# Kernel optimization log

Measured on AMD Instinct MI355X. Metric: run time of the kernel, lower is better.

## Reference

```python
import jax, jax.numpy as jnp
import numpy as np

N_NODES = 100000


def _gcn_norm(edge_index, num_nodes):
    # Add self-loops, then symmetric normalization D^-1/2 A D^-1/2 (PyG gcn_norm).
    loops = jnp.arange(num_nodes, dtype=edge_index.dtype)
    src = jnp.concatenate([edge_index[0], loops])
    dst = jnp.concatenate([edge_index[1], loops])
    ew = jnp.ones(src.shape[0], dtype=jnp.float32)
    deg = jax.ops.segment_sum(ew, dst, num_segments=num_nodes)
    dinv = jnp.where(deg > 0, jax.lax.rsqrt(deg), 0.0)
    norm = dinv[src] * ew * dinv[dst]
    return src, dst, norm


def _prop_gcn_conv(x, W, b, src, dst, norm, num_nodes, prop_nums):
    # PropGCNConv: linear transform once, then prop_nums hops of normalized
    # sparse propagation (gather from src, scale, scatter-add to dst), + bias.
    x = x @ W
    for _ in range(prop_nums):
        msgs = x[src] * norm[:, None]              # [E, d]
        x = jax.ops.segment_sum(msgs, dst, num_segments=num_nodes)
    return x + b


def setup_inputs() -> dict:
    key = jax.random.key(0)
    k1, k2, k3, k4 = jax.random.split(key, 4)
    in_dim, hid_dim, num_classes = 128, 64, 40
    n_edges = 800000
    x = jax.random.normal(k1, (N_NODES, in_dim), dtype=jnp.float32)
    W0 = jax.random.normal(k2, (in_dim, hid_dim), dtype=jnp.float32) * (1.0 / np.sqrt(in_dim))
    b0 = jnp.zeros((hid_dim,), dtype=jnp.float32)
    Wc = jax.random.normal(k3, (hid_dim, num_classes), dtype=jnp.float32) * (1.0 / np.sqrt(hid_dim))
    bc = jnp.zeros((num_classes,), dtype=jnp.float32)
    edge_index = jax.random.randint(k4, (2, n_edges), 0, N_NODES, dtype=jnp.int64)
    return {"x": x, "W0": W0, "b0": b0, "Wc": Wc, "bc": bc,
            "edge_index": edge_index, "prop_nums": 30}


def reference(x, W0, b0, Wc, bc, edge_index, prop_nums):
    n = x.shape[0]
    src, dst, norm = _gcn_norm(edge_index, n)
    # feat_bottleneck: conv -> relu -> dropout (eval mode -> identity)
    h = _prop_gcn_conv(x, W0, b0, src, dst, norm, n, prop_nums)
    h = jax.nn.relu(h)
    # feat_classifier: single-hop PropGCNConv
    out = _prop_gcn_conv(h, Wc, bc, src, dst, norm, n, 1)
    return out
```

## Files before the change

### kernel.cpp

```cpp
#include <hip/hip_runtime.h>

#define NN  100000
#define NE  800000
#define NNZ 900000
#define IN_DIM 128
#define HID 64
#define NC  40
#define HOPS 30
#define PB  2048
#define NPAIR (NN / 2)

typedef _Float16 half8 __attribute__((ext_vector_type(8)));


__global__ void count_edges_k(const int* __restrict__ dst, int* __restrict__ cnt) {
    int e = blockIdx.x * blockDim.x + threadIdx.x;
    if (e < NE) atomicAdd(&cnt[dst[e]], 1);
}

__global__ void dinv_k(const int* __restrict__ cnt, float* __restrict__ dinv) {
    int i = blockIdx.x * blockDim.x + threadIdx.x;
    if (i < NN) dinv[i] = rsqrtf((float)(cnt[i] + 1));
}

__global__ void scan_blocks_k(const int* __restrict__ cnt, int* __restrict__ rp,
                              int* __restrict__ partials) {
    __shared__ int s[256];
    int tid = threadIdx.x;
    int i = blockIdx.x * 256 + tid;
    int v = (i < NN) ? (cnt[i] + 1) : 0;
    s[tid] = v;
    __syncthreads();
    for (int off = 1; off < 256; off <<= 1) {
        int t = (tid >= off) ? s[tid - off] : 0;
        __syncthreads();
        s[tid] += t;
        __syncthreads();
    }
    if (i < NN) rp[i] = s[tid] - v;
    if (tid == 255) partials[blockIdx.x] = s[255];
}

__global__ void scan_partials_k(int* __restrict__ partials, int nblk) {
    __shared__ int s[512];
    int tid = threadIdx.x;
    int v = (tid < nblk) ? partials[tid] : 0;
    s[tid] = v;
    __syncthreads();
    for (int off = 1; off < 512; off <<= 1) {
        int t = (tid >= off) ? s[tid - off] : 0;
        __syncthreads();
        s[tid] += t;
        __syncthreads();
    }
    if (tid < nblk) partials[tid] = s[tid] - v;
}

__global__ void add_offsets_k(int* __restrict__ rp, const int* __restrict__ partials) {
    int i = blockIdx.x * 256 + threadIdx.x;
    if (i < NN) rp[i] += partials[blockIdx.x];
    if (i == 0) rp[NN] = NNZ;
}

__global__ void fill_csr_k(const int* __restrict__ src, const int* __restrict__ dst,
                           const float* __restrict__ dinv, const int* __restrict__ rp,
                           int* __restrict__ cnt, int2* __restrict__ cv) {
    int e = blockIdx.x * blockDim.x + threadIdx.x;
    if (e >= NNZ) return;
    int pos;
    int2 p;
    if (e < NE) {
        int s = src[e], d = dst[e];
        int old = atomicAdd(&cnt[d], -1);
        pos = rp[d] + old - 1;
        p.x = s;
        p.y = __float_as_int(dinv[s] * dinv[d]);
    } else {
        int i = e - NE;
        pos = rp[i + 1] - 1;
        p.x = i;
        p.y = __float_as_int(dinv[i] * dinv[i]);
    }
    cv[pos] = p;
}


__global__ void __launch_bounds__(256) gemm1_k(const float* __restrict__ x,
                                               const float* __restrict__ W,
                                               _Float16* __restrict__ out) {
    int t = threadIdx.x;
    int cq = __builtin_amdgcn_readfirstlane(t >> 6);
    int node = blockIdx.x * 64 + (t & 63);
    int nc = node < NN ? node : NN - 1;
    const float4* xr = (const float4*)(x + (size_t)nc * IN_DIM);
    const float* Wq = W + cq * 16;
    float acc[16];
#pragma unroll
    for (int c = 0; c < 16; ++c) acc[c] = 0.f;
#pragma unroll 4
    for (int k4 = 0; k4 < IN_DIM / 4; ++k4) {
        float4 xv = xr[k4];
#pragma unroll
        for (int kk = 0; kk < 4; ++kk) {
            float xs = (kk == 0) ? xv.x : (kk == 1) ? xv.y : (kk == 2) ? xv.z : xv.w;
            const float4* wr = (const float4*)(Wq + (k4 * 4 + kk) * HID);
#pragma unroll
            for (int c4 = 0; c4 < 4; ++c4) {
                float4 wv = wr[c4];
                acc[c4 * 4 + 0] = fmaf(xs, wv.x, acc[c4 * 4 + 0]);
                acc[c4 * 4 + 1] = fmaf(xs, wv.y, acc[c4 * 4 + 1]);
                acc[c4 * 4 + 2] = fmaf(xs, wv.z, acc[c4 * 4 + 2]);
                acc[c4 * 4 + 3] = fmaf(xs, wv.w, acc[c4 * 4 + 3]);
            }
        }
    }
    if (node < NN) {
        half8* o = (half8*)(out + (size_t)node * HID + cq * 16);
        half8 r0, r1;
#pragma unroll
        for (int j = 0; j < 8; ++j) {
            r0[j] = (_Float16)acc[j];
            r1[j] = (_Float16)acc[j + 8];
        }
        o[0] = r0;
        o[1] = r1;
    }
}

__global__ void __launch_bounds__(256) prop64_k(const _Float16* __restrict__ xin,
                                                _Float16* __restrict__ xout,
                                                const int* __restrict__ rp,
                                                const int2* __restrict__ cv) {
    int w    = (blockIdx.x * 256 + threadIdx.x) >> 6;
    int lane = threadIdx.x & 63;
    int n    = lane >> 5;
    int s    = (lane >> 3) & 3;
    int f    = lane & 7;
    const int NW = PB * 4;
    const half8* x8 = (const half8*)xin;
    for (int p = w; p < NPAIR; p += NW) {
        int node = p * 2 + n;
        int beg = rp[node], end = rp[node + 1];
        float a0 = 0.f, a1 = 0.f, a2 = 0.f, a3 = 0.f,
              a4 = 0.f, a5 = 0.f, a6 = 0.f, a7 = 0.f;
        for (int e = beg + s; e < end; e += 16) {
            int  e1 = e + 4,  e2 = e + 8,  e3 = e + 12;
            bool p1 = e1 < end, p2 = e2 < end, p3 = e3 < end;
            int2 q0 = cv[e];
            int2 q1 = cv[p1 ? e1 : beg];
            int2 q2 = cv[p2 ? e2 : beg];
            int2 q3 = cv[p3 ? e3 : beg];
            float v0 = __int_as_float(q0.y);
            float v1 = p1 ? __int_as_float(q1.y) : 0.f;
            float v2 = p2 ? __int_as_float(q2.y) : 0.f;
            float v3 = p3 ? __int_as_float(q3.y) : 0.f;
            half8 x0 = x8[(size_t)q0.x * 8 + f];
            half8 x1 = x8[(size_t)q1.x * 8 + f];
            half8 x2 = x8[(size_t)q2.x * 8 + f];
            half8 x3 = x8[(size_t)q3.x * 8 + f];
            a0 += v0 * (float)x0[0] + v1 * (float)x1[0] + v2 * (float)x2[0] + v3 * (float)x3[0];
            a1 += v0 * (float)x0[1] + v1 * (float)x1[1] + v2 * (float)x2[1] + v3 * (float)x3[1];
            a2 += v0 * (float)x0[2] + v1 * (float)x1[2] + v2 * (float)x2[2] + v3 * (float)x3[2];
            a3 += v0 * (float)x0[3] + v1 * (float)x1[3] + v2 * (float)x2[3] + v3 * (float)x3[3];
            a4 += v0 * (float)x0[4] + v1 * (float)x1[4] + v2 * (float)x2[4] + v3 * (float)x3[4];
            a5 += v0 * (float)x0[5] + v1 * (float)x1[5] + v2 * (float)x2[5] + v3 * (float)x3[5];
            a6 += v0 * (float)x0[6] + v1 * (float)x1[6] + v2 * (float)x2[6] + v3 * (float)x3[6];
            a7 += v0 * (float)x0[7] + v1 * (float)x1[7] + v2 * (float)x2[7] + v3 * (float)x3[7];
        }
#pragma unroll
        for (int m = 8; m <= 16; m <<= 1) {
            a0 += __shfl_xor(a0, m); a1 += __shfl_xor(a1, m);
            a2 += __shfl_xor(a2, m); a3 += __shfl_xor(a3, m);
            a4 += __shfl_xor(a4, m); a5 += __shfl_xor(a5, m);
            a6 += __shfl_xor(a6, m); a7 += __shfl_xor(a7, m);
        }
        if (s == 0) {
            half8 r;
            r[0] = (_Float16)a0; r[1] = (_Float16)a1; r[2] = (_Float16)a2; r[3] = (_Float16)a3;
            r[4] = (_Float16)a4; r[5] = (_Float16)a5; r[6] = (_Float16)a6; r[7] = (_Float16)a7;
            ((half8*)xout)[(size_t)node * 8 + f] = r;
        }
    }
}

__global__ void __launch_bounds__(256, 4) gemm2_k(const _Float16* __restrict__ h,
                                                  const float* __restrict__ b0,
                                                  const float* __restrict__ Wc,
                                                  _Float16* __restrict__ g) {
    __shared__ float Wcs[HID * NC];
    __shared__ float b0s[HID];
    int t = threadIdx.x;
    for (int i = t; i < HID * NC / 4; i += 256)
        ((float4*)Wcs)[i] = ((const float4*)Wc)[i];
    if (t < HID) b0s[t] = b0[t];
    __syncthreads();
    int node = blockIdx.x * 256 + t;
    if (node >= NN) return;
    const half8* hr = (const half8*)(h + (size_t)node * HID);
    float acc[NC];
#pragma unroll
    for (int c = 0; c < NC; ++c) acc[c] = 0.f;
#pragma unroll
    for (int j = 0; j < 8; ++j) {
        half8 hv = hr[j];
#pragma unroll
        for (int m = 0; m < 8; ++m) {
            int k = j * 8 + m;
            float fv = fmaxf((float)hv[m] + b0s[k], 0.f);
            const float4* wr = (const float4*)(Wcs + k * NC);
#pragma unroll
            for (int c4 = 0; c4 < NC / 4; ++c4) {
                float4 wv = wr[c4];
                acc[c4 * 4 + 0] = fmaf(fv, wv.x, acc[c4 * 4 + 0]);
                acc[c4 * 4 + 1] = fmaf(fv, wv.y, acc[c4 * 4 + 1]);
                acc[c4 * 4 + 2] = fmaf(fv, wv.z, acc[c4 * 4 + 2]);
                acc[c4 * 4 + 3] = fmaf(fv, wv.w, acc[c4 * 4 + 3]);
            }
        }
    }
    half8* go = (half8*)(g + (size_t)node * NC);
#pragma unroll
    for (int j = 0; j < 5; ++j) {
        half8 r;
#pragma unroll
        for (int m = 0; m < 8; ++m) r[m] = (_Float16)acc[j * 8 + m];
        go[j] = r;
    }
}

__global__ void __launch_bounds__(256) prop40_k(const _Float16* __restrict__ g,
                                                float* __restrict__ out,
                                                const int* __restrict__ rp,
                                                const int2* __restrict__ cv,
                                                const float* __restrict__ bc) {
    int w    = (blockIdx.x * 256 + threadIdx.x) >> 6;
    int lane = threadIdx.x & 63;
    int s = lane >> 3;
    int f = lane & 7;
    const int NW = PB * 4;
    const half8* g8 = (const half8*)g;
    bool act = f < 5;
    for (int node = w; node < NN; node += NW) {
        int beg = rp[node], end = rp[node + 1];
        float a0 = 0.f, a1 = 0.f, a2 = 0.f, a3 = 0.f, a4 = 0.f, a5 = 0.f, a6 = 0.f, a7 = 0.f;
        for (int e = beg + s; e < end; e += 16) {
            int  e1 = e + 8;
            bool p1 = e1 < end;
            int2 q0 = cv[e];
            int2 q1 = cv[p1 ? e1 : beg];
            float v0 = __int_as_float(q0.y);
            float v1 = p1 ? __int_as_float(q1.y) : 0.f;
            if (act) {
                half8 x0 = g8[(size_t)q0.x * 5 + f];
                half8 x1 = g8[(size_t)q1.x * 5 + f];
                a0 += v0 * (float)x0[0] + v1 * (float)x1[0];
                a1 += v0 * (float)x0[1] + v1 * (float)x1[1];
                a2 += v0 * (float)x0[2] + v1 * (float)x1[2];
                a3 += v0 * (float)x0[3] + v1 * (float)x1[3];
                a4 += v0 * (float)x0[4] + v1 * (float)x1[4];
                a5 += v0 * (float)x0[5] + v1 * (float)x1[5];
                a6 += v0 * (float)x0[6] + v1 * (float)x1[6];
                a7 += v0 * (float)x0[7] + v1 * (float)x1[7];
            }
        }
#pragma unroll
        for (int m = 8; m <= 32; m <<= 1) {
            a0 += __shfl_xor(a0, m); a1 += __shfl_xor(a1, m);
            a2 += __shfl_xor(a2, m); a3 += __shfl_xor(a3, m);
            a4 += __shfl_xor(a4, m); a5 += __shfl_xor(a5, m);
            a6 += __shfl_xor(a6, m); a7 += __shfl_xor(a7, m);
        }
        if (s == 0 && act) {
            float* o = out + (size_t)node * NC + f * 8;
            o[0] = a0 + bc[f * 8 + 0];
            o[1] = a1 + bc[f * 8 + 1];
            o[2] = a2 + bc[f * 8 + 2];
            o[3] = a3 + bc[f * 8 + 3];
            o[4] = a4 + bc[f * 8 + 4];
            o[5] = a5 + bc[f * 8 + 5];
            o[6] = a6 + bc[f * 8 + 6];
            o[7] = a7 + bc[f * 8 + 7];
        }
    }
}


extern "C" void kernel_launch(void* const* d_in, const int* in_sizes, int n_in,
                              void* d_out, int out_size, void* d_ws, size_t ws_size,
                              hipStream_t stream) {
    const float* x  = (const float*)d_in[0];
    const float* W0 = (const float*)d_in[1];
    const float* b0 = (const float*)d_in[2];
    const float* Wc = (const float*)d_in[3];
    const float* bc = (const float*)d_in[4];
    const int*   ei = (const int*)d_in[5];
    const int* src = ei;
    const int* dst = ei + NE;

    char* ws = (char*)d_ws;
    size_t off = 0;
    auto alloc = [&](size_t bytes) -> void* {
        void* p = ws + off;
        off = (off + bytes + 255) & ~(size_t)255;
        return p;
    };
    float* dinv     = (float*)alloc((size_t)NN * 4);
    int*   rp       = (int*)  alloc((size_t)(NN + 1) * 4);
    int*   cnt      = (int*)  alloc((size_t)NN * 4);
    int*   partials = (int*)  alloc(512 * 4);
    int2*  cvp      = (int2*) alloc((size_t)NNZ * 8);
    _Float16* XA    = (_Float16*)alloc((size_t)NN * HID * 2);
    _Float16* XB    = (_Float16*)alloc((size_t)NN * HID * 2);
    _Float16* G     = (_Float16*)alloc((size_t)NN * NC * 2);

    const int nblk_n = (NN + 255) / 256;

    hipMemsetAsync(cnt, 0, (size_t)NN * 4, stream);
    count_edges_k<<<(NE + 255) / 256, 256, 0, stream>>>(dst, cnt);
    dinv_k       <<<nblk_n, 256, 0, stream>>>(cnt, dinv);
    scan_blocks_k<<<nblk_n, 256, 0, stream>>>(cnt, rp, partials);
    scan_partials_k<<<1, 512, 0, stream>>>(partials, nblk_n);
    add_offsets_k<<<nblk_n, 256, 0, stream>>>(rp, partials);
    fill_csr_k   <<<(NNZ + 255) / 256, 256, 0, stream>>>(src, dst, dinv, rp, cnt, cvp);

    gemm1_k<<<(NN + 63) / 64, 256, 0, stream>>>(x, W0, XA);

    _Float16* a = XA;
    _Float16* b = XB;
    for (int hop = 0; hop < HOPS; ++hop) {
        prop64_k<<<PB, 256, 0, stream>>>(a, b, rp, cvp);
        _Float16* tmp = a; a = b; b = tmp;
    }

    gemm2_k<<<nblk_n, 256, 0, stream>>>(a, b0, Wc, G);
    prop40_k<<<PB, 256, 0, stream>>>(G, (float*)d_out, rp, cvp, bc);
}
```

Before: 880.3 us.

## Split hidden features into four 16-wide planes for cache-friendly propagation

Hidden activations move from node-major 64-wide rows to four feature-quarter planes of 16 halves each. Each propagation block handles one quarter, so the random gathers within a block hit a 3.2 MB plane that can stay cache resident. Block IDs are interleaved across quarters. Edge reads and output writes now use nontemporal hints, and gemm2 is reworked to read the new layout. In exchange, the CSR edge list is read four times per hop and each gather fetches only 32 bytes.

```diff
diff --git a/kernel.cpp b/kernel.cpp
--- a/kernel.cpp
+++ b/kernel.cpp
@@ -8,7 +8,6 @@
 #define NC  40
 #define HOPS 30
 #define PB  2048
-#define NPAIR (NN / 2)
 
 typedef _Float16 half8 __attribute__((ext_vector_type(8)));
 
@@ -115,7 +114,7 @@
         }
     }
     if (node < NN) {
-        half8* o = (half8*)(out + (size_t)node * HID + cq * 16);
+        half8* o = (half8*)out + ((size_t)cq * NN + node) * 2;
         half8 r0, r1;
 #pragma unroll
         for (int j = 0; j < 8; ++j) {
@@ -127,48 +126,49 @@
     }
 }
 
-__global__ void __launch_bounds__(256) prop64_k(const _Float16* __restrict__ xin,
-                                                _Float16* __restrict__ xout,
-                                                const int* __restrict__ rp,
-                                                const int2* __restrict__ cv) {
-    int w    = (blockIdx.x * 256 + threadIdx.x) >> 6;
+__global__ void __launch_bounds__(256, 8) prop16_k(const _Float16* __restrict__ xin,
+                                                   _Float16* __restrict__ xout,
+                                                   const int* __restrict__ rp,
+                                                   const int2* __restrict__ cv) {
+    int b = blockIdx.x;
+    int q = (b & 7) >> 1;
+    int j = ((b >> 3) << 1) | (b & 1);
+    int wid  = threadIdx.x >> 6;
     int lane = threadIdx.x & 63;
-    int n    = lane >> 5;
-    int s    = (lane >> 3) & 3;
-    int f    = lane & 7;
-    const int NW = PB * 4;
-    const half8* x8 = (const half8*)xin;
-    for (int p = w; p < NPAIR; p += NW) {
-        int node = p * 2 + n;
+    int n = lane >> 3;
+    int s = (lane >> 1) & 3;
+    int f = lane & 1;
+    const half8* x8 = (const half8*)xin + (size_t)q * NN * 2;
+    half8* o8 = (half8*)xout + (size_t)q * NN * 2;
+    const long long* cvl = (const long long*)cv;
+    for (int base = j * 32; base < NN; base += 512 * 32) {
+        int node = base + wid * 8 + n;
+        if (node >= NN) node = NN - 1;
         int beg = rp[node], end = rp[node + 1];
         float a0 = 0.f, a1 = 0.f, a2 = 0.f, a3 = 0.f,
               a4 = 0.f, a5 = 0.f, a6 = 0.f, a7 = 0.f;
-        for (int e = beg + s; e < end; e += 16) {
-            int  e1 = e + 4,  e2 = e + 8,  e3 = e + 12;
-            bool p1 = e1 < end, p2 = e2 < end, p3 = e3 < end;
-            int2 q0 = cv[e];
-            int2 q1 = cv[p1 ? e1 : beg];
-            int2 q2 = cv[p2 ? e2 : beg];
-            int2 q3 = cv[p3 ? e3 : beg];
-            float v0 = __int_as_float(q0.y);
-            float v1 = p1 ? __int_as_float(q1.y) : 0.f;
-            float v2 = p2 ? __int_as_float(q2.y) : 0.f;
-            float v3 = p3 ? __int_as_float(q3.y) : 0.f;
-            half8 x0 = x8[(size_t)q0.x * 8 + f];
-            half8 x1 = x8[(size_t)q1.x * 8 + f];
-            half8 x2 = x8[(size_t)q2.x * 8 + f];
-            half8 x3 = x8[(size_t)q3.x * 8 + f];
-            a0 += v0 * (float)x0[0] + v1 * (float)x1[0] + v2 * (float)x2[0] + v3 * (float)x3[0];
-            a1 += v0 * (float)x0[1] + v1 * (float)x1[1] + v2 * (float)x2[1] + v3 * (float)x3[1];
-            a2 += v0 * (float)x0[2] + v1 * (float)x1[2] + v2 * (float)x2[2] + v3 * (float)x3[2];
-            a3 += v0 * (float)x0[3] + v1 * (float)x1[3] + v2 * (float)x2[3] + v3 * (float)x3[3];
-            a4 += v0 * (float)x0[4] + v1 * (float)x1[4] + v2 * (float)x2[4] + v3 * (float)x3[4];
-            a5 += v0 * (float)x0[5] + v1 * (float)x1[5] + v2 * (float)x2[5] + v3 * (float)x3[5];
-            a6 += v0 * (float)x0[6] + v1 * (float)x1[6] + v2 * (float)x2[6] + v3 * (float)x3[6];
-            a7 += v0 * (float)x0[7] + v1 * (float)x1[7] + v2 * (float)x2[7] + v3 * (float)x3[7];
-        }
-#pragma unroll
-        for (int m = 8; m <= 16; m <<= 1) {
+        for (int e = beg + s; e < end; e += 8) {
+            int  e1 = e + 4;
+            bool p1 = e1 < end;
+            long long L0 = __builtin_nontemporal_load(cvl + e);
+            long long L1 = __builtin_nontemporal_load(cvl + (p1 ? e1 : e));
+            int c0 = (int)L0;
+            int c1 = (int)L1;
+            float v0 = __int_as_float((int)(L0 >> 32));
+            float v1 = p1 ? __int_as_float((int)(L1 >> 32)) : 0.f;
+            half8 xa = x8[(size_t)c0 * 2 + f];
+            half8 xb = x8[(size_t)c1 * 2 + f];
+            a0 += v0 * (float)xa[0] + v1 * (float)xb[0];
+            a1 += v0 * (float)xa[1] + v1 * (float)xb[1];
+            a2 += v0 * (float)xa[2] + v1 * (float)xb[2];
+            a3 += v0 * (float)xa[3] + v1 * (float)xb[3];
+            a4 += v0 * (float)xa[4] + v1 * (float)xb[4];
+            a5 += v0 * (float)xa[5] + v1 * (float)xb[5];
+            a6 += v0 * (float)xa[6] + v1 * (float)xb[6];
+            a7 += v0 * (float)xa[7] + v1 * (float)xb[7];
+        }
+#pragma unroll
+        for (int m = 2; m <= 4; m <<= 1) {
             a0 += __shfl_xor(a0, m); a1 += __shfl_xor(a1, m);
             a2 += __shfl_xor(a2, m); a3 += __shfl_xor(a3, m);
             a4 += __shfl_xor(a4, m); a5 += __shfl_xor(a5, m);
@@ -178,15 +178,15 @@
             half8 r;
             r[0] = (_Float16)a0; r[1] = (_Float16)a1; r[2] = (_Float16)a2; r[3] = (_Float16)a3;
             r[4] = (_Float16)a4; r[5] = (_Float16)a5; r[6] = (_Float16)a6; r[7] = (_Float16)a7;
-            ((half8*)xout)[(size_t)node * 8 + f] = r;
-        }
-    }
-}
-
-__global__ void __launch_bounds__(256, 4) gemm2_k(const _Float16* __restrict__ h,
-                                                  const float* __restrict__ b0,
-                                                  const float* __restrict__ Wc,
-                                                  _Float16* __restrict__ g) {
+            __builtin_nontemporal_store(r, &o8[(size_t)node * 2 + f]);
+        }
+    }
+}
+
+__global__ void __launch_bounds__(256) gemm2_k(const _Float16* __restrict__ h,
+                                               const float* __restrict__ b0,
+                                               const float* __restrict__ Wc,
+                                               _Float16* __restrict__ g) {
     __shared__ float Wcs[HID * NC];
     __shared__ float b0s[HID];
     int t = threadIdx.x;
@@ -194,37 +194,36 @@
         ((float4*)Wcs)[i] = ((const float4*)Wc)[i];
     if (t < HID) b0s[t] = b0[t];
     __syncthreads();
-    int node = blockIdx.x * 256 + t;
+    int cq = __builtin_amdgcn_readfirstlane(t >> 6);
+    int node = blockIdx.x * 64 + (t & 63);
     if (node >= NN) return;
-    const half8* hr = (const half8*)(h + (size_t)node * HID);
-    float acc[NC];
-#pragma unroll
-    for (int c = 0; c < NC; ++c) acc[c] = 0.f;
-#pragma unroll
-    for (int j = 0; j < 8; ++j) {
-        half8 hv = hr[j];
-#pragma unroll
-        for (int m = 0; m < 8; ++m) {
-            int k = j * 8 + m;
-            float fv = fmaxf((float)hv[m] + b0s[k], 0.f);
-            const float4* wr = (const float4*)(Wcs + k * NC);
-#pragma unroll
-            for (int c4 = 0; c4 < NC / 4; ++c4) {
-                float4 wv = wr[c4];
-                acc[c4 * 4 + 0] = fmaf(fv, wv.x, acc[c4 * 4 + 0]);
-                acc[c4 * 4 + 1] = fmaf(fv, wv.y, acc[c4 * 4 + 1]);
-                acc[c4 * 4 + 2] = fmaf(fv, wv.z, acc[c4 * 4 + 2]);
-                acc[c4 * 4 + 3] = fmaf(fv, wv.w, acc[c4 * 4 + 3]);
+    const half8* hq = (const half8*)h;
+    float acc[10];
+#pragma unroll
+    for (int c = 0; c < 10; ++c) acc[c] = 0.f;
+#pragma unroll
+    for (int q = 0; q < 4; ++q) {
+#pragma unroll
+        for (int jj = 0; jj < 2; ++jj) {
+            half8 hv = hq[((size_t)q * NN + node) * 2 + jj];
+#pragma unroll
+            for (int m = 0; m < 8; ++m) {
+                int k = q * 16 + jj * 8 + m;
+                float fv = fmaxf((float)hv[m] + b0s[k], 0.f);
+                const float* wr = Wcs + k * NC + cq * 10;
+#pragma unroll
+                for (int c = 0; c < 10; ++c)
+                    acc[c] = fmaf(fv, wr[c], acc[c]);
             }
         }
     }
-    half8* go = (half8*)(g + (size_t)node * NC);
-#pragma unroll
-    for (int j = 0; j < 5; ++j) {
-        half8 r;
-#pragma unroll
-        for (int m = 0; m < 8; ++m) r[m] = (_Float16)acc[j * 8 + m];
-        go[j] = r;
+    unsigned* go = (unsigned*)((char*)g + (size_t)node * 80 + cq * 20);
+#pragma unroll
+    for (int i = 0; i < 5; ++i) {
+        union { _Float16 hh[2]; unsigned u; } u;
+        u.hh[0] = (_Float16)acc[2 * i];
+        u.hh[1] = (_Float16)acc[2 * i + 1];
+        go[i] = u.u;
     }
 }
 
@@ -314,6 +313,7 @@
     _Float16* G     = (_Float16*)alloc((size_t)NN * NC * 2);
 
     const int nblk_n = (NN + 255) / 256;
+    const int nblk64 = (NN + 63) / 64;
 
     hipMemsetAsync(cnt, 0, (size_t)NN * 4, stream);
     count_edges_k<<<(NE + 255) / 256, 256, 0, stream>>>(dst, cnt);
@@ -323,15 +323,15 @@
     add_offsets_k<<<nblk_n, 256, 0, stream>>>(rp, partials);
     fill_csr_k   <<<(NNZ + 255) / 256, 256, 0, stream>>>(src, dst, dinv, rp, cnt, cvp);
 
-    gemm1_k<<<(NN + 63) / 64, 256, 0, stream>>>(x, W0, XA);
+    gemm1_k<<<nblk64, 256, 0, stream>>>(x, W0, XA);
 
     _Float16* a = XA;
     _Float16* b = XB;
     for (int hop = 0; hop < HOPS; ++hop) {
-        prop64_k<<<PB, 256, 0, stream>>>(a, b, rp, cvp);
+        prop16_k<<<PB, 256, 0, stream>>>(a, b, rp, cvp);
         _Float16* tmp = a; a = b; b = tmp;
     }
 
-    gemm2_k<<<nblk_n, 256, 0, stream>>>(a, b0, Wc, G);
+    gemm2_k<<<nblk64, 256, 0, stream>>>(a, b0, Wc, G);
     prop40_k<<<PB, 256, 0, stream>>>(G, (float*)d_out, rp, cvp, bc);
 }
```

New measurement: 1.524 ms. 73.1% more time.
